# Kernel optimization log

Measured on AMD Instinct MI355X. Metric: run time of the kernel, lower is better.

The kernel has to match this reference:

```python
import jax, jax.numpy as jnp
import numpy as np

N_NODES = 50000
N_EDGES = 1600000
N_GRAPHS = 256
IN_CH = 128
HID = 128
OUT_CH = 10


def gcn_conv(x, W, b, src, dst, ew, num_nodes):
    # PyG GCNConv: add self-loops (weight 1), symmetric deg^-1/2 normalization,
    # linear transform first, aggregate via scatter-add, bias after.
    loop = jnp.arange(num_nodes)
    s = jnp.concatenate([src, loop])
    d = jnp.concatenate([dst, loop])
    w = jnp.concatenate([ew, jnp.ones((num_nodes,), x.dtype)])
    deg = jax.ops.segment_sum(w, d, num_segments=num_nodes)
    dinv = jnp.where(deg > 0, jax.lax.rsqrt(deg), 0.0)
    norm = dinv[s] * dinv[d] * w                     # [E+N]
    h = x @ W                                        # [N, H]
    msg = h[s] * norm[:, None]                       # gather + scale
    out = jax.ops.segment_sum(msg, d, num_segments=num_nodes)  # scatter-add
    return out + b


def setup_inputs() -> dict:
    key = jax.random.key(0)
    ks = jax.random.split(key, 12)
    x = jax.random.normal(ks[0], (N_NODES, IN_CH), jnp.float32)
    edge_index = jax.random.randint(ks[1], (2, N_EDGES), 0, N_NODES, jnp.int64)
    edge_weight = jax.random.uniform(ks[2], (N_EDGES,), jnp.float32)
    batch = jnp.sort(jax.random.randint(ks[3], (N_NODES,), 0, N_GRAPHS, jnp.int64))
    s = 1.0 / np.sqrt(HID)
    W1 = jax.random.normal(ks[4], (IN_CH, HID), jnp.float32) / np.sqrt(IN_CH)
    b1 = jnp.zeros((HID,), jnp.float32)
    W2 = jax.random.normal(ks[5], (HID, HID), jnp.float32) * s
    b2 = jnp.zeros((HID,), jnp.float32)
    W3 = jax.random.normal(ks[6], (HID, HID), jnp.float32) * s
    b3 = jnp.zeros((HID,), jnp.float32)
    lw1 = jax.random.normal(ks[7], (HID, HID), jnp.float32) * s
    lb1 = jax.random.normal(ks[8], (HID,), jnp.float32) * s
    lw2 = jax.random.normal(ks[9], (HID, OUT_CH), jnp.float32) * s
    lb2 = jax.random.normal(ks[10], (OUT_CH,), jnp.float32) * s
    return {"x": x, "edge_index": edge_index, "edge_weight": edge_weight,
            "batch": batch, "W1": W1, "b1": b1, "W2": W2, "b2": b2,
            "W3": W3, "b3": b3, "lw1": lw1, "lb1": lb1, "lw2": lw2, "lb2": lb2}


def reference(x, edge_index, edge_weight, batch, W1, b1, W2, b2, W3, b3, lw1, lb1, lw2, lb2):
    src, dst = edge_index[0], edge_index[1]
    h = jax.nn.relu(gcn_conv(x, W1, b1, src, dst, edge_weight, N_NODES))
    h = jax.nn.relu(gcn_conv(h, W2, b2, src, dst, edge_weight, N_NODES))
    h = gcn_conv(h, W3, b3, src, dst, edge_weight, N_NODES)
    # global mean pool over graphs
    sums = jax.ops.segment_sum(h, batch, num_segments=N_GRAPHS)
    cnt = jax.ops.segment_sum(jnp.ones((N_NODES,), h.dtype), batch, num_segments=N_GRAPHS)
    emb = sums / jnp.maximum(cnt, 1.0)[:, None]      # [G, HID]
    out = (emb @ lw1 + lb1) @ lw2 + lb2              # classify: lin1 -> lin2
    return out
```

## Files before the change

### kernel.cpp

```cpp
#include <hip/hip_runtime.h>

#define N_NODES 50000
#define N_EDGES 1600000
#define N_GRAPHS 256
#define HID 128
#define OUT_CH 10
#define PAD 80
#define NBUCK 512
#define BNODES ((N_NODES + NBUCK - 1) / NBUCK)
#define BCAP 6144
#define P1BLK 250
#define EPB (N_EDGES / P1BLK)
#define DSENTINEL 127
#define NR 4
#define RSTEP ((N_NODES + NR - 1) / NR)

typedef __bf16 bf16x8 __attribute__((ext_vector_type(8)));
typedef float f32x4 __attribute__((ext_vector_type(4)));

__device__ inline unsigned bf16rne(float f) {
    unsigned u = __float_as_uint(f);
    return (u + 0x7fffu + ((u >> 16) & 1u)) >> 16;
}

__global__ __launch_bounds__(1024) void bucket_k(const int* __restrict__ src,
                                                 const int* __restrict__ dst,
                                                 const float* __restrict__ ew,
                                                 int* __restrict__ bcount,
                                                 int2* __restrict__ cpair) {
    __shared__ int hist[NBUCK];
    __shared__ int base[NBUCK];
    int t = threadIdx.x;
    for (int i = t; i < NBUCK; i += 1024) hist[i] = 0;
    __syncthreads();
    const int ch0 = blockIdx.x * (EPB / 4);
    const int ch1 = ch0 + (EPB / 4);
    const int4* dst4 = (const int4*)dst;
    const int4* src4 = (const int4*)src;
    const float4* ew4 = (const float4*)ew;
    for (int ci = ch0 + t; ci < ch1; ci += 1024) {
        int4 d4 = dst4[ci];
        atomicAdd(&hist[d4.x / BNODES], 1);
        atomicAdd(&hist[d4.y / BNODES], 1);
        atomicAdd(&hist[d4.z / BNODES], 1);
        atomicAdd(&hist[d4.w / BNODES], 1);
    }
    __syncthreads();
    for (int i = t; i < NBUCK; i += 1024) {
        int c = hist[i];
        base[i] = (c > 0) ? atomicAdd(&bcount[i], (c + 7) & ~7) : 0;
        hist[i] = 0;
    }
    __syncthreads();
    for (int ci = ch0 + t; ci < ch1; ci += 1024) {
        int4 d4 = dst4[ci];
        int4 s4 = src4[ci];
        float4 w4 = ew4[ci];
#define PROC(dd, ss, ww)                                          \
        {                                                         \
            int b = (dd) / BNODES;                                \
            int off = base[b] + atomicAdd(&hist[b], 1);           \
            if (off < BCAP) {                                     \
                int2 p;                                           \
                p.x = (((dd) - b * BNODES) << 16) | (ss);         \
                p.y = __float_as_int(ww);                         \
                cpair[b * BCAP + off] = p;                        \
            }                                                     \
        }
        PROC(d4.x, s4.x, w4.x)
        PROC(d4.y, s4.y, w4.y)
        PROC(d4.z, s4.z, w4.z)
        PROC(d4.w, s4.w, w4.w)
#undef PROC
    }
    __syncthreads();
    for (int i = t; i < NBUCK; i += 1024) {
        int c = hist[i];
        int ac = (c + 7) & ~7;
        for (int j = c; j < ac; ++j) {
            int off = base[i] + j;
            if (off < BCAP) {
                int2 p;
                p.x = DSENTINEL << 16;
                p.y = 0;
                cpair[i * BCAP + off] = p;
            }
        }
    }
}

__global__ __launch_bounds__(512) void ell_scatter_k(const int* __restrict__ bcount,
                                                     const int2* __restrict__ cpair,
                                                     int2* __restrict__ ell,
                                                     int* __restrict__ fill,
                                                     float* __restrict__ dinv) {
    __shared__ int lcnt[BNODES * NR];
    __shared__ float wsum[BNODES];
    int b = blockIdx.x;
    int t = threadIdx.x;
    for (int i = t; i < BNODES * NR; i += 512) lcnt[i] = 0;
    for (int i = t; i < BNODES; i += 512) wsum[i] = 0.f;
    __syncthreads();
    int cnt = bcount[b];
    if (cnt > BCAP) cnt = BCAP;
    int n0 = b * BNODES;
    int sbase = b * BCAP;
    for (int i = t; i < cnt; i += 512) {
        int2 p = cpair[sbase + i];
        int dloc = p.x >> 16;
        if (dloc < BNODES) {
            int r = (p.x & 0xffff) / RSTEP;
            atomicAdd(&lcnt[dloc * NR + r], 1);
            atomicAdd(&wsum[dloc], __int_as_float(p.y));
        }
    }
    __syncthreads();
    for (int i = t; i < BNODES; i += 512) {
        int c0 = lcnt[i * NR + 0], c1 = lcnt[i * NR + 1];
        int c2 = lcnt[i * NR + 2], c3 = lcnt[i * NR + 3];
        int total = c0 + c1 + c2 + c3;
        lcnt[i * NR + 0] = 0;
        lcnt[i * NR + 1] = c0;
        lcnt[i * NR + 2] = c0 + c1;
        lcnt[i * NR + 3] = c0 + c1 + c2;
        int n = n0 + i;
        if (n < N_NODES) {
            fill[n] = total < PAD ? total : PAD;
            dinv[n] = rsqrtf(wsum[i] + 1.0f);
        }
    }
    __syncthreads();
    for (int i = t; i < cnt; i += 512) {
        int2 p = cpair[sbase + i];
        int dloc = p.x >> 16;
        if (dloc < BNODES) {
            int s = p.x & 0xffff;
            int r = s / RSTEP;
            int pos = atomicAdd(&lcnt[dloc * NR + r], 1);
            if (pos < PAD) {
                int2 q;
                q.x = s;
                q.y = p.y;
                ell[(size_t)(n0 + dloc) * PAD + pos] = q;
            }
        }
    }
}

__global__ __launch_bounds__(256) void prep_k(const int* __restrict__ batch,
                                              int* __restrict__ gstart,
                                              const float* __restrict__ W1,
                                              const float* __restrict__ W2,
                                              const float* __restrict__ W3,
                                              unsigned short* __restrict__ Wt) {
    int idx = blockIdx.x * 256 + threadIdx.x;
    if (idx < 3 * 16384) {
        int m = idx >> 14;
        int r = idx & 16383;
        const float* W = (m == 0) ? W1 : (m == 1) ? W2 : W3;
        int c = r >> 7, k = r & 127;
        Wt[idx] = (unsigned short)bf16rne(W[k * 128 + c]);
    }
    if (idx < N_NODES) {
        int b = batch[idx];
        int bprev = (idx == 0) ? -1 : batch[idx - 1];
        for (int g = bprev + 1; g <= b; ++g) gstart[g] = idx;
        if (idx == N_NODES - 1) {
            for (int g = b + 1; g <= N_GRAPHS; ++g) gstart[g] = N_NODES;
        }
    }
}

__global__ __launch_bounds__(256) void gemm_mfma_k(const float* __restrict__ A32,
                                                   const unsigned short* __restrict__ Ab,
                                                   const unsigned short* __restrict__ Wt,
                                                   unsigned short* __restrict__ Cb,
                                                   int n_rows) {
    int tid = threadIdx.x;
    int wave = tid >> 6;
    int lane = tid & 63;
    int m = lane & 15;
    int quad = lane >> 4;
    int row = blockIdx.x * 64 + wave * 16 + m;
    int rowc = row < n_rows ? row : n_rows - 1;
    f32x4 acc[8] = {};
#pragma unroll
    for (int kc = 0; kc < 4; ++kc) {
        bf16x8 a;
        if (A32) {
            const float4* Ar = (const float4*)(A32 + (size_t)rowc * 128 + kc * 32 + quad * 8);
            float4 lo = Ar[0], hi = Ar[1];
            union { bf16x8 v; unsigned short s[8]; } u;
            u.s[0] = (unsigned short)bf16rne(lo.x);
            u.s[1] = (unsigned short)bf16rne(lo.y);
            u.s[2] = (unsigned short)bf16rne(lo.z);
            u.s[3] = (unsigned short)bf16rne(lo.w);
            u.s[4] = (unsigned short)bf16rne(hi.x);
            u.s[5] = (unsigned short)bf16rne(hi.y);
            u.s[6] = (unsigned short)bf16rne(hi.z);
            u.s[7] = (unsigned short)bf16rne(hi.w);
            a = u.v;
        } else {
            a = *(const bf16x8*)(Ab + (size_t)rowc * 128 + kc * 32 + quad * 8);
        }
#pragma unroll
        for (int ct = 0; ct < 8; ++ct) {
            bf16x8 b = *(const bf16x8*)(Wt + (size_t)(ct * 16 + m) * 128 + kc * 32 + quad * 8);
            acc[ct] = __builtin_amdgcn_mfma_f32_16x16x32_bf16(a, b, acc[ct], 0, 0, 0);
        }
    }
    int obase = blockIdx.x * 64 + wave * 16 + quad * 4;
#pragma unroll
    for (int ct = 0; ct < 8; ++ct) {
#pragma unroll
        for (int r = 0; r < 4; ++r) {
            int n = obase + r;
            if (n < n_rows)
                Cb[(size_t)n * 128 + ct * 16 + m] = (unsigned short)bf16rne(acc[ct][r]);
        }
    }
}

__global__ __launch_bounds__(256) void agg_k(const unsigned short* __restrict__ tb,
                                             const int* __restrict__ fill,
                                             const int2* __restrict__ ell,
                                             const float* __restrict__ dinv,
                                             const float* __restrict__ bias,
                                             unsigned short* __restrict__ outB, int relu) {
    int lane = threadIdx.x & 15;
    int local = threadIdx.x >> 4;
    int n = blockIdx.x * 16 + local;
    if (n >= N_NODES) return;
    float dn = dinv[n];
#define UNP(q, f)                                                 \
    float f##0 = __uint_as_float((q).x << 16);                    \
    float f##1 = __uint_as_float((q).x & 0xffff0000u);            \
    float f##2 = __uint_as_float((q).y << 16);                    \
    float f##3 = __uint_as_float((q).y & 0xffff0000u);            \
    float f##4 = __uint_as_float((q).z << 16);                    \
    float f##5 = __uint_as_float((q).z & 0xffff0000u);            \
    float f##6 = __uint_as_float((q).w << 16);                    \
    float f##7 = __uint_as_float((q).w & 0xffff0000u);
    uint4 qs = ((const uint4*)(tb + (size_t)n * 128))[lane];
    UNP(qs, s)
    float acc0 = s0 * dn, acc1 = s1 * dn, acc2 = s2 * dn, acc3 = s3 * dn;
    float acc4 = s4 * dn, acc5 = s5 * dn, acc6 = s6 * dn, acc7 = s7 * dn;
    const int2* ep = ell + (size_t)n * PAD;
    int c = fill[n];
    int i = 0;
    for (; i + 4 <= c; i += 4) {
        int2 p0 = ep[i], p1 = ep[i + 1], p2 = ep[i + 2], p3 = ep[i + 3];
        uint4 q0 = ((const uint4*)(tb + (size_t)p0.x * 128))[lane];
        uint4 q1 = ((const uint4*)(tb + (size_t)p1.x * 128))[lane];
        uint4 q2 = ((const uint4*)(tb + (size_t)p2.x * 128))[lane];
        uint4 q3 = ((const uint4*)(tb + (size_t)p3.x * 128))[lane];
        float w0 = __int_as_float(p0.y) * dinv[p0.x];
        float w1 = __int_as_float(p1.y) * dinv[p1.x];
        float w2 = __int_as_float(p2.y) * dinv[p2.x];
        float w3 = __int_as_float(p3.y) * dinv[p3.x];
        UNP(q0, a)
        UNP(q1, b)
        UNP(q2, cc)
        UNP(q3, d)
        acc0 += a0 * w0 + b0 * w1 + cc0 * w2 + d0 * w3;
        acc1 += a1 * w0 + b1 * w1 + cc1 * w2 + d1 * w3;
        acc2 += a2 * w0 + b2 * w1 + cc2 * w2 + d2 * w3;
        acc3 += a3 * w0 + b3 * w1 + cc3 * w2 + d3 * w3;
        acc4 += a4 * w0 + b4 * w1 + cc4 * w2 + d4 * w3;
        acc5 += a5 * w0 + b5 * w1 + cc5 * w2 + d5 * w3;
        acc6 += a6 * w0 + b6 * w1 + cc6 * w2 + d6 * w3;
        acc7 += a7 * w0 + b7 * w1 + cc7 * w2 + d7 * w3;
    }
    for (; i < c; ++i) {
        int2 p = ep[i];
        float w = __int_as_float(p.y) * dinv[p.x];
        uint4 q = ((const uint4*)(tb + (size_t)p.x * 128))[lane];
        UNP(q, a)
        acc0 += a0 * w; acc1 += a1 * w; acc2 += a2 * w; acc3 += a3 * w;
        acc4 += a4 * w; acc5 += a5 * w; acc6 += a6 * w; acc7 += a7 * w;
    }
#undef UNP
    float4 b0 = ((const float4*)bias)[lane * 2];
    float4 b1 = ((const float4*)bias)[lane * 2 + 1];
    acc0 = acc0 * dn + b0.x; acc1 = acc1 * dn + b0.y;
    acc2 = acc2 * dn + b0.z; acc3 = acc3 * dn + b0.w;
    acc4 = acc4 * dn + b1.x; acc5 = acc5 * dn + b1.y;
    acc6 = acc6 * dn + b1.z; acc7 = acc7 * dn + b1.w;
    if (relu) {
        acc0 = fmaxf(acc0, 0.f); acc1 = fmaxf(acc1, 0.f);
        acc2 = fmaxf(acc2, 0.f); acc3 = fmaxf(acc3, 0.f);
        acc4 = fmaxf(acc4, 0.f); acc5 = fmaxf(acc5, 0.f);
        acc6 = fmaxf(acc6, 0.f); acc7 = fmaxf(acc7, 0.f);
    }
    uint4 pk;
    pk.x = bf16rne(acc0) | (bf16rne(acc1) << 16);
    pk.y = bf16rne(acc2) | (bf16rne(acc3) << 16);
    pk.z = bf16rne(acc4) | (bf16rne(acc5) << 16);
    pk.w = bf16rne(acc6) | (bf16rne(acc7) << 16);
    ((uint4*)(outB + (size_t)n * 128))[lane] = pk;
}

#define PCHUNK 49
__global__ __launch_bounds__(128) void pool1_k(const unsigned short* __restrict__ hb,
                                               const int* __restrict__ batch,
                                               float* __restrict__ pool) {
    int c = threadIdx.x;
    int n0 = blockIdx.x * PCHUNK;
    if (n0 >= N_NODES) return;
    int n1 = n0 + PCHUNK;
    if (n1 > N_NODES) n1 = N_NODES;
    int g = batch[n0];
    float run = 0.f;
    for (int n = n0; n < n1; ++n) {
        int gn = batch[n];
        if (gn != g) {
            atomicAdd(&pool[g * 128 + c], run);
            run = 0.f;
            g = gn;
        }
        run += __uint_as_float((unsigned)hb[(size_t)n * 128 + c] << 16);
    }
    atomicAdd(&pool[g * 128 + c], run);
}

__global__ __launch_bounds__(128) void cls2_k(const float* __restrict__ pool,
                                              const int* __restrict__ gstart,
                                              const float* __restrict__ lw1,
                                              const float* __restrict__ lb1,
                                              const float* __restrict__ lw2,
                                              const float* __restrict__ lb2,
                                              float* __restrict__ out) {
    __shared__ float emb[128];
    __shared__ float mid[128];
    int g = blockIdx.x, c = threadIdx.x;
    float cntf = fmaxf((float)(gstart[g + 1] - gstart[g]), 1.0f);
    emb[c] = pool[(size_t)g * 128 + c] / cntf;
    __syncthreads();
    float a = lb1[c];
    for (int k = 0; k < 128; ++k) a += emb[k] * lw1[k * 128 + c];
    mid[c] = a;
    __syncthreads();
    if (c < OUT_CH) {
        float o = lb2[c];
        for (int k = 0; k < 128; ++k) o += mid[k] * lw2[k * OUT_CH + c];
        out[g * OUT_CH + c] = o;
    }
}

extern "C" void kernel_launch(void* const* d_in, const int* in_sizes, int n_in,
                              void* d_out, int out_size, void* d_ws, size_t ws_size,
                              hipStream_t stream) {
    const float* x = (const float*)d_in[0];
    const int* ei = (const int*)d_in[1];
    const int* src = ei;
    const int* dst = ei + N_EDGES;
    const float* ew = (const float*)d_in[2];
    const int* batch = (const int*)d_in[3];
    const float* W1 = (const float*)d_in[4];
    const float* b1 = (const float*)d_in[5];
    const float* W2 = (const float*)d_in[6];
    const float* b2 = (const float*)d_in[7];
    const float* W3 = (const float*)d_in[8];
    const float* b3 = (const float*)d_in[9];
    const float* lw1 = (const float*)d_in[10];
    const float* lb1 = (const float*)d_in[11];
    const float* lw2 = (const float*)d_in[12];
    const float* lb2 = (const float*)d_in[13];
    float* out = (float*)d_out;

    char* ws = (char*)d_ws;
    size_t off = 0;
    auto alloc = [&](size_t bytes) {
        size_t cur = off;
        off += (bytes + 255) & ~(size_t)255;
        return cur;
    };
    size_t o_bcount = alloc(NBUCK * 4);
    size_t o_pool = alloc(N_GRAPHS * HID * 4);
    size_t zero_end = off;
    size_t o_fill = alloc(N_NODES * 4);
    size_t o_dinv = alloc(N_NODES * 4);
    size_t o_gstart = alloc((N_GRAPHS + 1) * 4);
    size_t o_wt = alloc(3 * 16384 * 2);
    size_t o_ell = alloc((size_t)N_NODES * PAD * 8);
    size_t o_cpair = alloc((size_t)NBUCK * BCAP * 8);
    size_t o_gAb = alloc((size_t)N_NODES * HID * 2);
    size_t o_aggB = alloc((size_t)N_NODES * HID * 2);
    (void)ws_size;

    int* bcount = (int*)(ws + o_bcount);
    float* pool = (float*)(ws + o_pool);
    int* fill = (int*)(ws + o_fill);
    float* dinv = (float*)(ws + o_dinv);
    int* gstart = (int*)(ws + o_gstart);
    unsigned short* Wt = (unsigned short*)(ws + o_wt);
    int2* ell = (int2*)(ws + o_ell);
    int2* cpair = (int2*)(ws + o_cpair);
    unsigned short* gAb = (unsigned short*)(ws + o_gAb);
    unsigned short* aggB = (unsigned short*)(ws + o_aggB);

    hipMemsetAsync(d_ws, 0, zero_end, stream);

    bucket_k<<<P1BLK, 1024, 0, stream>>>(src, dst, ew, bcount, cpair);
    ell_scatter_k<<<NBUCK, 512, 0, stream>>>(bcount, cpair, ell, fill, dinv);
    prep_k<<<196, 256, 0, stream>>>(batch, gstart, W1, W2, W3, Wt);

    int gemm_blocks = (N_NODES + 63) / 64;
    int agg_blocks = (N_NODES + 15) / 16;
    gemm_mfma_k<<<gemm_blocks, 256, 0, stream>>>(x, (const unsigned short*)0, Wt, gAb, N_NODES);
    agg_k<<<agg_blocks, 256, 0, stream>>>(gAb, fill, ell, dinv, b1, aggB, 1);
    gemm_mfma_k<<<gemm_blocks, 256, 0, stream>>>((const float*)0, aggB, Wt + 16384, gAb, N_NODES);
    agg_k<<<agg_blocks, 256, 0, stream>>>(gAb, fill, ell, dinv, b2, aggB, 1);
    gemm_mfma_k<<<gemm_blocks, 256, 0, stream>>>((const float*)0, aggB, Wt + 32768, gAb, N_NODES);
    agg_k<<<agg_blocks, 256, 0, stream>>>(gAb, fill, ell, dinv, b3, aggB, 0);

    pool1_k<<<(N_NODES + PCHUNK - 1) / PCHUNK, 128, 0, stream>>>(aggB, batch, pool);
    cls2_k<<<N_GRAPHS, 128, 0, stream>>>(pool, gstart, lw1, lb1, lw2, lb2, out);
}
```

Measured before the change: 389.9 us.

## Pack ELL entries into 32-bit words with prescaled bf16 weights

Each ELL entry goes from int2 (source index plus fp32 weight) to one 32-bit word holding a 16-bit source index and a bf16 weight. A new kernel premultiplies each edge weight by dinv[src], which removes the per-edge dinv gather from all three aggregation passes. Aggregation now reads edges as uint4 vectors and unrolls by 8 for more memory-level parallelism. The cost is an extra kernel launch and a pass over the ELL array, plus bf16 rounding of the normalized weights, which loses some accuracy.

```diff
diff --git a/kernel.cpp b/kernel.cpp
--- a/kernel.cpp
+++ b/kernel.cpp
@@ -91,7 +91,7 @@
 
 __global__ __launch_bounds__(512) void ell_scatter_k(const int* __restrict__ bcount,
                                                      const int2* __restrict__ cpair,
-                                                     int2* __restrict__ ell,
+                                                     unsigned* __restrict__ ell,
                                                      int* __restrict__ fill,
                                                      float* __restrict__ dinv) {
     __shared__ int lcnt[BNODES * NR];
@@ -137,13 +137,25 @@
             int s = p.x & 0xffff;
             int r = s / RSTEP;
             int pos = atomicAdd(&lcnt[dloc * NR + r], 1);
-            if (pos < PAD) {
-                int2 q;
-                q.x = s;
-                q.y = p.y;
-                ell[(size_t)(n0 + dloc) * PAD + pos] = q;
-            }
-        }
+            if (pos < PAD)
+                ell[(size_t)(n0 + dloc) * PAD + pos] =
+                    (bf16rne(__int_as_float(p.y)) << 16) | (unsigned)s;
+        }
+    }
+}
+
+__global__ __launch_bounds__(256) void scale_w_k(unsigned* __restrict__ ell,
+                                                 const int* __restrict__ fill,
+                                                 const float* __restrict__ dinv) {
+    int idx = blockIdx.x * blockDim.x + threadIdx.x;
+    if (idx >= N_NODES * PAD) return;
+    int n = idx / PAD;
+    int j = idx - n * PAD;
+    if (j < fill[n]) {
+        unsigned e = ell[idx];
+        int s = e & 0xffff;
+        float w = __uint_as_float(e & 0xffff0000u) * dinv[s];
+        ell[idx] = (bf16rne(w) << 16) | (unsigned)s;
     }
 }
 
@@ -223,7 +235,7 @@
 
 __global__ __launch_bounds__(256) void agg_k(const unsigned short* __restrict__ tb,
                                              const int* __restrict__ fill,
-                                             const int2* __restrict__ ell,
+                                             const unsigned* __restrict__ ell,
                                              const float* __restrict__ dinv,
                                              const float* __restrict__ bias,
                                              unsigned short* __restrict__ outB, int relu) {
@@ -241,44 +253,66 @@
     float f##5 = __uint_as_float((q).z & 0xffff0000u);            \
     float f##6 = __uint_as_float((q).w << 16);                    \
     float f##7 = __uint_as_float((q).w & 0xffff0000u);
+#define EDGE(e, s, w)                                             \
+    int s = (e) & 0xffff;                                         \
+    float w = __uint_as_float((e) & 0xffff0000u);
     uint4 qs = ((const uint4*)(tb + (size_t)n * 128))[lane];
     UNP(qs, s)
     float acc0 = s0 * dn, acc1 = s1 * dn, acc2 = s2 * dn, acc3 = s3 * dn;
     float acc4 = s4 * dn, acc5 = s5 * dn, acc6 = s6 * dn, acc7 = s7 * dn;
-    const int2* ep = ell + (size_t)n * PAD;
+    const uint4* ep4 = (const uint4*)(ell + (size_t)n * PAD);
     int c = fill[n];
     int i = 0;
+    for (; i + 8 <= c; i += 8) {
+        uint4 eA = ep4[i >> 2];
+        uint4 eB = ep4[(i >> 2) + 1];
+        EDGE(eA.x, sA0, wA0) EDGE(eA.y, sA1, wA1) EDGE(eA.z, sA2, wA2) EDGE(eA.w, sA3, wA3)
+        EDGE(eB.x, sB0, wB0) EDGE(eB.y, sB1, wB1) EDGE(eB.z, sB2, wB2) EDGE(eB.w, sB3, wB3)
+        uint4 q0 = ((const uint4*)(tb + (size_t)sA0 * 128))[lane];
+        uint4 q1 = ((const uint4*)(tb + (size_t)sA1 * 128))[lane];
+        uint4 q2 = ((const uint4*)(tb + (size_t)sA2 * 128))[lane];
+        uint4 q3 = ((const uint4*)(tb + (size_t)sA3 * 128))[lane];
+        uint4 q4 = ((const uint4*)(tb + (size_t)sB0 * 128))[lane];
+        uint4 q5 = ((const uint4*)(tb + (size_t)sB1 * 128))[lane];
+        uint4 q6 = ((const uint4*)(tb + (size_t)sB2 * 128))[lane];
+        uint4 q7 = ((const uint4*)(tb + (size_t)sB3 * 128))[lane];
+        UNP(q0, a) UNP(q1, b) UNP(q2, cc) UNP(q3, d)
+        UNP(q4, e) UNP(q5, f) UNP(q6, g) UNP(q7, h)
+        acc0 += a0 * wA0 + b0 * wA1 + cc0 * wA2 + d0 * wA3 + e0 * wB0 + f0 * wB1 + g0 * wB2 + h0 * wB3;
+        acc1 += a1 * wA0 + b1 * wA1 + cc1 * wA2 + d1 * wA3 + e1 * wB0 + f1 * wB1 + g1 * wB2 + h1 * wB3;
+        acc2 += a2 * wA0 + b2 * wA1 + cc2 * wA2 + d2 * wA3 + e2 * wB0 + f2 * wB1 + g2 * wB2 + h2 * wB3;
+        acc3 += a3 * wA0 + b3 * wA1 + cc3 * wA2 + d3 * wA3 + e3 * wB0 + f3 * wB1 + g3 * wB2 + h3 * wB3;
+        acc4 += a4 * wA0 + b4 * wA1 + cc4 * wA2 + d4 * wA3 + e4 * wB0 + f4 * wB1 + g4 * wB2 + h4 * wB3;
+        acc5 += a5 * wA0 + b5 * wA1 + cc5 * wA2 + d5 * wA3 + e5 * wB0 + f5 * wB1 + g5 * wB2 + h5 * wB3;
+        acc6 += a6 * wA0 + b6 * wA1 + cc6 * wA2 + d6 * wA3 + e6 * wB0 + f6 * wB1 + g6 * wB2 + h6 * wB3;
+        acc7 += a7 * wA0 + b7 * wA1 + cc7 * wA2 + d7 * wA3 + e7 * wB0 + f7 * wB1 + g7 * wB2 + h7 * wB3;
+    }
     for (; i + 4 <= c; i += 4) {
-        int2 p0 = ep[i], p1 = ep[i + 1], p2 = ep[i + 2], p3 = ep[i + 3];
-        uint4 q0 = ((const uint4*)(tb + (size_t)p0.x * 128))[lane];
-        uint4 q1 = ((const uint4*)(tb + (size_t)p1.x * 128))[lane];
-        uint4 q2 = ((const uint4*)(tb + (size_t)p2.x * 128))[lane];
-        uint4 q3 = ((const uint4*)(tb + (size_t)p3.x * 128))[lane];
-        float w0 = __int_as_float(p0.y) * dinv[p0.x];
-        float w1 = __int_as_float(p1.y) * dinv[p1.x];
-        float w2 = __int_as_float(p2.y) * dinv[p2.x];
-        float w3 = __int_as_float(p3.y) * dinv[p3.x];
-        UNP(q0, a)
-        UNP(q1, b)
-        UNP(q2, cc)
-        UNP(q3, d)
-        acc0 += a0 * w0 + b0 * w1 + cc0 * w2 + d0 * w3;
-        acc1 += a1 * w0 + b1 * w1 + cc1 * w2 + d1 * w3;
-        acc2 += a2 * w0 + b2 * w1 + cc2 * w2 + d2 * w3;
-        acc3 += a3 * w0 + b3 * w1 + cc3 * w2 + d3 * w3;
-        acc4 += a4 * w0 + b4 * w1 + cc4 * w2 + d4 * w3;
-        acc5 += a5 * w0 + b5 * w1 + cc5 * w2 + d5 * w3;
-        acc6 += a6 * w0 + b6 * w1 + cc6 * w2 + d6 * w3;
-        acc7 += a7 * w0 + b7 * w1 + cc7 * w2 + d7 * w3;
+        uint4 eA = ep4[i >> 2];
+        EDGE(eA.x, sA0, wA0) EDGE(eA.y, sA1, wA1) EDGE(eA.z, sA2, wA2) EDGE(eA.w, sA3, wA3)
+        uint4 q0 = ((const uint4*)(tb + (size_t)sA0 * 128))[lane];
+        uint4 q1 = ((const uint4*)(tb + (size_t)sA1 * 128))[lane];
+        uint4 q2 = ((const uint4*)(tb + (size_t)sA2 * 128))[lane];
+        uint4 q3 = ((const uint4*)(tb + (size_t)sA3 * 128))[lane];
+        UNP(q0, a) UNP(q1, b) UNP(q2, cc) UNP(q3, d)
+        acc0 += a0 * wA0 + b0 * wA1 + cc0 * wA2 + d0 * wA3;
+        acc1 += a1 * wA0 + b1 * wA1 + cc1 * wA2 + d1 * wA3;
+        acc2 += a2 * wA0 + b2 * wA1 + cc2 * wA2 + d2 * wA3;
+        acc3 += a3 * wA0 + b3 * wA1 + cc3 * wA2 + d3 * wA3;
+        acc4 += a4 * wA0 + b4 * wA1 + cc4 * wA2 + d4 * wA3;
+        acc5 += a5 * wA0 + b5 * wA1 + cc5 * wA2 + d5 * wA3;
+        acc6 += a6 * wA0 + b6 * wA1 + cc6 * wA2 + d6 * wA3;
+        acc7 += a7 * wA0 + b7 * wA1 + cc7 * wA2 + d7 * wA3;
     }
     for (; i < c; ++i) {
-        int2 p = ep[i];
-        float w = __int_as_float(p.y) * dinv[p.x];
-        uint4 q = ((const uint4*)(tb + (size_t)p.x * 128))[lane];
+        unsigned e = ell[(size_t)n * PAD + i];
+        EDGE(e, s, w)
+        uint4 q = ((const uint4*)(tb + (size_t)s * 128))[lane];
         UNP(q, a)
         acc0 += a0 * w; acc1 += a1 * w; acc2 += a2 * w; acc3 += a3 * w;
         acc4 += a4 * w; acc5 += a5 * w; acc6 += a6 * w; acc7 += a7 * w;
     }
+#undef EDGE
 #undef UNP
     float4 b0 = ((const float4*)bias)[lane * 2];
     float4 b1 = ((const float4*)bias)[lane * 2 + 1];
@@ -382,7 +416,7 @@
     size_t o_dinv = alloc(N_NODES * 4);
     size_t o_gstart = alloc((N_GRAPHS + 1) * 4);
     size_t o_wt = alloc(3 * 16384 * 2);
-    size_t o_ell = alloc((size_t)N_NODES * PAD * 8);
+    size_t o_ell = alloc((size_t)N_NODES * PAD * 4);
     size_t o_cpair = alloc((size_t)NBUCK * BCAP * 8);
     size_t o_gAb = alloc((size_t)N_NODES * HID * 2);
     size_t o_aggB = alloc((size_t)N_NODES * HID * 2);
@@ -394,7 +428,7 @@
     float* dinv = (float*)(ws + o_dinv);
     int* gstart = (int*)(ws + o_gstart);
     unsigned short* Wt = (unsigned short*)(ws + o_wt);
-    int2* ell = (int2*)(ws + o_ell);
+    unsigned* ell = (unsigned*)(ws + o_ell);
     int2* cpair = (int2*)(ws + o_cpair);
     unsigned short* gAb = (unsigned short*)(ws + o_gAb);
     unsigned short* aggB = (unsigned short*)(ws + o_aggB);
@@ -403,6 +437,7 @@
 
     bucket_k<<<P1BLK, 1024, 0, stream>>>(src, dst, ew, bcount, cpair);
     ell_scatter_k<<<NBUCK, 512, 0, stream>>>(bcount, cpair, ell, fill, dinv);
+    scale_w_k<<<(N_NODES * PAD + 255) / 256, 256, 0, stream>>>(ell, fill, dinv);
     prep_k<<<196, 256, 0, stream>>>(batch, gstart, W1, W2, W3, Wt);
 
     int gemm_blocks = (N_NODES + 63) / 64;
```

New measurement: 386.5 us. Within noise of the previous version (-0.9%).
